# Performance work log

Measured on AMD Instinct MI355X. Metric: run time of the kernel, lower is better.

The kernel has to match this reference:

```python
import jax, jax.numpy as jnp
import numpy as np

B, S, D, H, DK, DV, SEG = 2, 4096, 1024, 8, 128, 128, 512
NSEG = S // SEG


def setup_inputs() -> dict:
    key = jax.random.key(0)
    k0, k1, k2, k3, k4, k5 = jax.random.split(key, 6)
    return {
        "x": jax.random.normal(k0, (B, S, D), jnp.float32),
        "Wk": jax.random.normal(k1, (H, D, DK), jnp.float32) / np.float32(np.sqrt(D)),
        "Wv": jax.random.normal(k2, (H, D, DV), jnp.float32) / np.float32(np.sqrt(D)),
        "Wq": jax.random.normal(k3, (H, D, DK), jnp.float32) / np.float32(np.sqrt(D)),
        "Wout": jax.random.normal(k4, (H * DV, D), jnp.float32) / np.float32(np.sqrt(H * DV)),
        "betas": jax.random.normal(k5, (1, H, 1, DV), jnp.float32),
    }


def reference(x, Wk, Wv, Wq, Wout, betas):
    # Per-head projections: (B,H,S,dk/dv)
    k_full = jnp.einsum('bsd,hdk->bhsk', x, Wk)
    v_full = jnp.einsum('bsd,hdk->bhsk', x, Wv)
    q_full = jnp.einsum('bsd,hdk->bhsk', x, Wq)

    def to_segs(t):  # (B,H,S,E) -> (NSEG,B,H,SEG,E)
        return t.reshape(B, H, NSEG, SEG, t.shape[-1]).transpose(2, 0, 1, 3, 4)

    segs = (to_segs(k_full), to_segs(v_full), to_segs(q_full))

    mem0 = jnp.zeros((B, H, DK, DV), x.dtype)           # compressive memory
    z0 = jnp.full((B, H, DK, 1), 1.0 / DK, x.dtype)     # normalizer
    causal_mask = jnp.tril(jnp.ones((SEG, SEG), bool))
    gate = jax.nn.sigmoid(betas)                        # (1,H,1,DV)
    scale = jnp.asarray(1.0 / np.sqrt(DK), x.dtype)

    def step(carry, seg):
        mem, z = carry
        k, v, q = seg                                   # (B,H,SEG,dk/dv)
        sigma_q = jax.nn.elu(q) + 1.0
        # segment-local causal softmax attention
        scores = jnp.einsum('bhik,bhjk->bhij', q, k) * scale
        scores = jnp.where(causal_mask, scores, -jnp.inf)
        att_dot = jax.nn.softmax(scores, axis=-1) @ v
        # linear-attention read from memory
        att_mem = (sigma_q @ mem) / (sigma_q @ z)
        # delta-rule memory update
        sigma_k = jax.nn.elu(k) + 1.0
        mem = mem + jnp.einsum('bhsk,bhsv->bhkv', sigma_k, v - (sigma_k @ mem) / (sigma_k @ z))
        z = z + jnp.sum(sigma_k, axis=-2, keepdims=True).swapaxes(-1, -2)
        # gated mix of memory and local attention
        att = gate * att_mem + (1.0 - gate) * att_dot   # (B,H,SEG,DV)
        att = att.transpose(0, 2, 1, 3).reshape(B, SEG, H * DV)
        return (mem, z), att @ Wout                     # (B,SEG,D)

    _, outs = jax.lax.scan(step, (mem0, z0), segs)      # (NSEG,B,SEG,D)
    return outs.transpose(1, 0, 2, 3).reshape(B, S, D)
```

## Files before the change

### kernel.cpp

```cpp
#include <hip/hip_runtime.h>

#define B_  2
#define S_  4096
#define D_  1024
#define H_  8
#define DK_ 128
#define DV_ 128
#define SEG_ 512
#define NSEG_ 8
#define BH_ 16
#define M_ 8192

typedef __attribute__((ext_vector_type(8))) short bf16x8;
typedef __attribute__((ext_vector_type(4))) float f32x4;

__device__ __forceinline__ float elu1(float x) { return x > 0.f ? x + 1.f : __expf(x); }
__device__ __forceinline__ float sigmoidf(float x) { return 1.f / (1.f + __expf(-x)); }

__device__ __forceinline__ unsigned short f2b(float f) {
    union { float f; unsigned int u; } x; x.f = f;
    unsigned int r = x.u + 0x7fffu + ((x.u >> 16) & 1u);
    return (unsigned short)(r >> 16);
}
__device__ __forceinline__ float b2f(unsigned short u) {
    union { unsigned int u; float f; } x; x.u = ((unsigned int)u) << 16; return x.f;
}

__device__ __forceinline__ void gl2lds16(const void* g, void* l) {
    __builtin_amdgcn_global_load_lds(
        (const __attribute__((address_space(1))) void*)g,
        (__attribute__((address_space(3))) void*)l, 16, 0, 0);
}

__global__ __launch_bounds__(256) void conv_bf16(
    const float* __restrict__ src, unsigned short* __restrict__ dst)
{
    int i = (blockIdx.x * 256 + threadIdx.x) * 4;
    float4 v = *(const float4*)(src + i);
    ushort4 o;
    o.x = f2b(v.x); o.y = f2b(v.y); o.z = f2b(v.z); o.w = f2b(v.w);
    *(ushort4*)(dst + i) = o;
}

__global__ __launch_bounds__(256) void transpose_conv(
    const float* __restrict__ src, unsigned short* __restrict__ dst, int R, int C)
{
    __shared__ float tile[32][33];
    const size_t moff = (size_t)blockIdx.z * R * C;
    src += moff; dst += moff;
    const int c0 = blockIdx.x * 32, r0 = blockIdx.y * 32;
    const int tx = threadIdx.x & 31, ty = threadIdx.x >> 5;
    #pragma unroll
    for (int i = 0; i < 32; i += 8)
        tile[ty + i][tx] = src[(size_t)(r0 + ty + i) * C + c0 + tx];
    __syncthreads();
    #pragma unroll
    for (int i = 0; i < 32; i += 8)
        dst[(size_t)(c0 + ty + i) * R + r0 + tx] = f2b(tile[tx][ty + i]);
}

__global__ __launch_bounds__(256) void colsum_k(
    const unsigned short* __restrict__ Kbb, float* __restrict__ colsum)
{
    __shared__ float red[32][128];
    const int t = threadIdx.x;
    const int bh = blockIdx.x >> 3, seg = blockIdx.x & 7;
    const unsigned short* Kp = Kbb + ((size_t)bh * 4096 + seg * 512) * 128;
    const int rbase = t >> 3, c0 = (t & 7) * 16;
    float part[16] = {};
    for (int chunk = 0; chunk < 16; ++chunk) {
        const unsigned short* p = Kp + (size_t)(chunk * 32 + rbase) * 128 + c0;
        bf16x8 a = *(const bf16x8*)p;
        bf16x8 b = *(const bf16x8*)(p + 8);
        #pragma unroll
        for (int j = 0; j < 8; ++j) {
            part[j]     += elu1(b2f((unsigned short)a[j]));
            part[j + 8] += elu1(b2f((unsigned short)b[j]));
        }
    }
    #pragma unroll
    for (int j = 0; j < 16; ++j) red[rbase][c0 + j] = part[j];
    __syncthreads();
    if (t < 128) {
        float s = 0.f;
        #pragma unroll
        for (int r = 0; r < 32; ++r) s += red[r][t];
        colsum[(size_t)blockIdx.x * 128 + t] = s;
    }
}

__global__ __launch_bounds__(256) void den_z(
    const unsigned short* __restrict__ Kbb, const float* __restrict__ colsum,
    float* __restrict__ den, float* __restrict__ zseg)
{
    __shared__ float zs[128];
    const int t = threadIdx.x;
    const int bh = blockIdx.x >> 3, seg = blockIdx.x & 7;
    if (t < 128) {
        float z = 1.f / 128.f;
        for (int j = 0; j < seg; ++j) z += colsum[(size_t)(bh * 8 + j) * 128 + t];
        zs[t] = z;
        zseg[(size_t)blockIdx.x * 128 + t] = z;
    }
    __syncthreads();
    #pragma unroll
    for (int rr = 0; rr < 2; ++rr) {
        int s = t + rr * 256;
        const unsigned short* kp = Kbb + ((size_t)bh * 4096 + seg * 512 + s) * 128;
        float d = 0.f;
        #pragma unroll 4
        for (int f = 0; f < 16; ++f) {
            bf16x8 a = *(const bf16x8*)(kp + f * 8);
            #pragma unroll
            for (int j = 0; j < 8; ++j)
                d += elu1(b2f((unsigned short)a[j])) * zs[f * 8 + j];
        }
        den[(size_t)bh * 4096 + seg * 512 + s] = d;
    }
}

__global__ __launch_bounds__(256) void sigma_kT2(
    const unsigned short* __restrict__ Kbb, const float* __restrict__ den,
    unsigned short* __restrict__ SkT, unsigned short* __restrict__ SkTs)
{
    __shared__ float tile[32][33];
    __shared__ float rden[32];
    const int bh = blockIdx.z;
    const int s0 = blockIdx.x * 32, dk0 = blockIdx.y * 32;
    const int tx = threadIdx.x & 31, ty = threadIdx.x >> 5;
    if (threadIdx.x < 32) rden[threadIdx.x] = 1.f / den[(size_t)bh * 4096 + s0 + threadIdx.x];
    #pragma unroll
    for (int i = 0; i < 32; i += 8)
        tile[ty + i][tx] = elu1(b2f(Kbb[((size_t)bh * 4096 + s0 + ty + i) * 128 + dk0 + tx]));
    __syncthreads();
    #pragma unroll
    for (int i = 0; i < 32; i += 8) {
        float v = tile[tx][ty + i];
        size_t o = ((size_t)bh * 128 + dk0 + ty + i) * 4096 + s0 + tx;
        SkT[o]  = f2b(v);
        SkTs[o] = f2b(v * rden[tx]);
    }
}

__device__ __forceinline__ void mfma_gemm_128(
    const unsigned short* __restrict__ A, int lda,
    const unsigned short* __restrict__ Bt, int ldb, int K,
    unsigned short* As, unsigned short* Bs, f32x4 acc[4][4])
{
    const int tid = threadIdx.x;
    const int wave = tid >> 6, lane = tid & 63;
    const int r4 = lane >> 2, c4 = (lane & 3) * 8;
    const int lrow = lane & 15, lquad = lane >> 4;
    const int wm = (wave >> 1) * 64, wn = (wave & 1) * 64;
    for (int k0 = 0; k0 < K; k0 += 32) {
        #pragma unroll
        for (int i = 0; i < 2; ++i) {
            int ar = wave * 32 + i * 16;
            gl2lds16(A  + (size_t)(ar + r4) * lda + k0 + c4, As + ar * 32);
            gl2lds16(Bt + (size_t)(ar + r4) * ldb + k0 + c4, Bs + ar * 32);
        }
        __syncthreads();
        bf16x8 af[4], bfr[4];
        #pragma unroll
        for (int i = 0; i < 4; ++i)
            af[i] = *(const bf16x8*)(As + (wm + i * 16 + lrow) * 32 + lquad * 8);
        #pragma unroll
        for (int j = 0; j < 4; ++j)
            bfr[j] = *(const bf16x8*)(Bs + (wn + j * 16 + lrow) * 32 + lquad * 8);
        #pragma unroll
        for (int i = 0; i < 4; ++i)
            #pragma unroll
            for (int j = 0; j < 4; ++j)
                acc[i][j] = __builtin_amdgcn_mfma_f32_16x16x32_bf16(af[i], bfr[j], acc[i][j], 0, 0, 0);
        __syncthreads();
    }
}

__global__ __launch_bounds__(256) void gemm_qkv_mfma(
    const unsigned short* __restrict__ xb, const unsigned short* __restrict__ Wtb,
    unsigned short* __restrict__ Qbb, unsigned short* __restrict__ Kbb,
    unsigned short* __restrict__ Vtb)
{
    __shared__ unsigned short As[128 * 32];
    __shared__ unsigned short Bs[128 * 32];
    const int m0 = blockIdx.x * 128;
    const int panel = blockIdx.y;
    const int which = panel >> 3, h = panel & 7;
    f32x4 acc[4][4] = {};
    mfma_gemm_128(xb + (size_t)m0 * 1024, 1024,
                  Wtb + (size_t)panel * 128 * 1024, 1024, 1024, As, Bs, acc);
    const int tid = threadIdx.x, wave = tid >> 6, lane = tid & 63;
    const int lrow = lane & 15, lquad = lane >> 4;
    const int wm = (wave >> 1) * 64, wn = (wave & 1) * 64;
    #pragma unroll
    for (int i = 0; i < 4; ++i)
        #pragma unroll
        for (int r = 0; r < 4; ++r) {
            int m = m0 + wm + i * 16 + lquad * 4 + r;
            int bb = m >> 12, s = m & 4095;
            int bh = bb * 8 + h;
            size_t rowbase = ((size_t)bh * 4096 + s) * 128;
            #pragma unroll
            for (int j = 0; j < 4; ++j) {
                int col = wn + j * 16 + lrow;
                unsigned short v = f2b(acc[i][j][r]);
                if (which == 0) Kbb[rowbase + col] = v;
                else if (which == 1)
                    Vtb[(((size_t)bh * 8 + (s >> 9)) * 128 + col) * 512 + (s & 511)] = v;
                else Qbb[rowbase + col] = v;
            }
        }
}

__global__ __launch_bounds__(256) void gemm_out_mfma(
    const unsigned short* __restrict__ A, const unsigned short* __restrict__ Bt,
    float* __restrict__ C)
{
    __shared__ unsigned short As[128 * 32];
    __shared__ unsigned short Bs[128 * 32];
    const int m0 = blockIdx.x * 128, n0 = blockIdx.y * 128;
    f32x4 acc[4][4] = {};
    mfma_gemm_128(A + (size_t)m0 * 1024, 1024,
                  Bt + (size_t)n0 * 1024, 1024, 1024, As, Bs, acc);
    const int tid = threadIdx.x, wave = tid >> 6, lane = tid & 63;
    const int lrow = lane & 15, lquad = lane >> 4;
    const int wm = (wave >> 1) * 64, wn = (wave & 1) * 64;
    #pragma unroll
    for (int i = 0; i < 4; ++i)
        #pragma unroll
        for (int r = 0; r < 4; ++r) {
            int m = m0 + wm + i * 16 + lquad * 4 + r;
            #pragma unroll
            for (int j = 0; j < 4; ++j)
                C[(size_t)m * 1024 + n0 + wn + j * 16 + lrow] = acc[i][j][r];
        }
}

__global__ __launch_bounds__(256) void ac_gemm(
    const unsigned short* __restrict__ SkT, const unsigned short* __restrict__ SkTs,
    const unsigned short* __restrict__ Vtb,
    unsigned short* __restrict__ Emat, float* __restrict__ Cmat)
{
    __shared__ unsigned short As[128 * 32];
    __shared__ unsigned short Bs1[128 * 32];
    __shared__ unsigned short Bs2[128 * 32];
    const int bh = blockIdx.x >> 3, seg = blockIdx.x & 7;
    const unsigned short* Ap  = SkT  + (size_t)bh * 128 * 4096 + seg * 512;
    const unsigned short* B1p = SkTs + (size_t)bh * 128 * 4096 + seg * 512;
    const unsigned short* B2p = Vtb  + (size_t)blockIdx.x * 128 * 512;
    const int tid = threadIdx.x;
    const int wave = tid >> 6, lane = tid & 63;
    const int r4 = lane >> 2, c4 = (lane & 3) * 8;
    const int lrow = lane & 15, lquad = lane >> 4;
    const int wm = (wave >> 1) * 64, wn = (wave & 1) * 64;
    f32x4 e[4][4] = {}, c[4][4] = {};
    for (int k0 = 0; k0 < 512; k0 += 32) {
        #pragma unroll
        for (int i = 0; i < 2; ++i) {
            int ar = wave * 32 + i * 16;
            gl2lds16(Ap  + (size_t)(ar + r4) * 4096 + k0 + c4, As  + ar * 32);
            gl2lds16(B1p + (size_t)(ar + r4) * 4096 + k0 + c4, Bs1 + ar * 32);
            gl2lds16(B2p + (size_t)(ar + r4) * 512  + k0 + c4, Bs2 + ar * 32);
        }
        __syncthreads();
        bf16x8 af[4], b1[4], b2[4];
        #pragma unroll
        for (int i = 0; i < 4; ++i)
            af[i] = *(const bf16x8*)(As + (wm + i * 16 + lrow) * 32 + lquad * 8);
        #pragma unroll
        for (int j = 0; j < 4; ++j) {
            b1[j] = *(const bf16x8*)(Bs1 + (wn + j * 16 + lrow) * 32 + lquad * 8);
            b2[j] = *(const bf16x8*)(Bs2 + (wn + j * 16 + lrow) * 32 + lquad * 8);
        }
        #pragma unroll
        for (int i = 0; i < 4; ++i)
            #pragma unroll
            for (int j = 0; j < 4; ++j) {
                e[i][j] = __builtin_amdgcn_mfma_f32_16x16x32_bf16(af[i], b1[j], e[i][j], 0, 0, 0);
                c[i][j] = __builtin_amdgcn_mfma_f32_16x16x32_bf16(af[i], b2[j], c[i][j], 0, 0, 0);
            }
        __syncthreads();
    }
    #pragma unroll
    for (int i = 0; i < 4; ++i)
        #pragma unroll
        for (int r = 0; r < 4; ++r) {
            int m = wm + i * 16 + lquad * 4 + r;
            #pragma unroll
            for (int j = 0; j < 4; ++j) {
                int nn = wn + j * 16 + lrow;
                size_t o = (size_t)blockIdx.x * 16384 + (size_t)m * 128 + nn;
                Emat[o] = f2b(-e[i][j][r]);
                Cmat[o] = c[i][j][r];
            }
        }
}

__global__ __launch_bounds__(512) void scan_step(
    const unsigned short* __restrict__ Emat, const float* __restrict__ Cmat,
    unsigned short* __restrict__ Memb)
{
    __shared__ unsigned short msh[128][136];
    const int t = threadIdx.x;
    const int wv = t >> 6, lane = t & 63;
    const int n16 = lane & 15, quad = lane >> 4;
    const int bh = blockIdx.x;
    f32x4 macc[8] = {};
    for (int seg = 0; seg < 8; ++seg) {
        unsigned short* gm = Memb + ((size_t)(bh * 8 + seg)) * 16384;
        #pragma unroll
        for (int vt = 0; vt < 8; ++vt) {
            ushort4 o;
            o.x = f2b(macc[vt][0]); o.y = f2b(macc[vt][1]);
            o.z = f2b(macc[vt][2]); o.w = f2b(macc[vt][3]);
            *(ushort4*)&msh[vt * 16 + n16][wv * 16 + quad * 4] = o;
            *(ushort4*)(gm + (size_t)(vt * 16 + n16) * 128 + wv * 16 + quad * 4) = o;
        }
        if (seg == 7) break;
        __syncthreads();
        const unsigned short* Ep = Emat + ((size_t)(bh * 8 + seg)) * 16384
                                 + (size_t)(wv * 16 + n16) * 128;
        bf16x8 ea[4];
        #pragma unroll
        for (int kf = 0; kf < 4; ++kf)
            ea[kf] = *(const bf16x8*)(Ep + kf * 32 + quad * 8);
        const float* Cp = Cmat + ((size_t)(bh * 8 + seg)) * 16384
                        + (size_t)(wv * 16 + quad * 4) * 128;
        #pragma unroll
        for (int vt = 0; vt < 8; ++vt)
            #pragma unroll
            for (int r = 0; r < 4; ++r)
                macc[vt][r] += Cp[(size_t)r * 128 + vt * 16 + n16];
        #pragma unroll
        for (int vt = 0; vt < 8; ++vt)
            #pragma unroll
            for (int kf = 0; kf < 4; ++kf) {
                bf16x8 bfr = *(const bf16x8*)&msh[vt * 16 + n16][kf * 32 + quad * 8];
                macc[vt] = __builtin_amdgcn_mfma_f32_16x16x32_bf16(ea[kf], bfr, macc[vt], 0, 0, 0);
            }
        __syncthreads();
    }
}

__global__ __launch_bounds__(256) void attn_out(
    const unsigned short* __restrict__ Qbb, const unsigned short* __restrict__ Kbb,
    const unsigned short* __restrict__ Vtb, const unsigned short* __restrict__ Memb,
    const float* __restrict__ zseg, const float* __restrict__ betas,
    unsigned short* __restrict__ Attb)
{
    __shared__ unsigned short Pl[4][16][72];
    const int tid = threadIdx.x, wave = tid >> 6, lane = tid & 63;
    const int n = lane & 15, quad = lane >> 4;
    const int bh = blockIdx.x >> 3, seg = blockIdx.x & 7, qt = blockIdx.y;
    const int b = bh >> 3, h = bh & 7;
    const float scale = 0.08838834764831845f;

    const unsigned short* Qp = Qbb + ((size_t)bh * 4096 + seg * 512 + qt * 64 + wave * 16) * 128;
    const unsigned short* Kp = Kbb + ((size_t)bh * 4096 + seg * 512) * 128;
    const unsigned short* Vp = Vtb + ((size_t)bh * 8 + seg) * 128 * 512;

    bf16x8 aQ[4];
    #pragma unroll
    for (int kc = 0; kc < 4; ++kc)
        aQ[kc] = *(const bf16x8*)(Qp + n * 128 + kc * 32 + quad * 8);

    f32x4 O[8] = {};
    float m_i[4], l_i[4];
    #pragma unroll
    for (int r = 0; r < 4; ++r) { m_i[r] = -1e30f; l_i[r] = 0.f; }

    for (int jt = 0; jt <= qt; ++jt) {
        f32x4 Sf[4] = {};
        #pragma unroll
        for (int kc = 0; kc < 4; ++kc) {
            bf16x8 bK[4];
            #pragma unroll
            for (int ns = 0; ns < 4; ++ns)
                bK[ns] = *(const bf16x8*)(Kp + (size_t)(jt * 64 + ns * 16 + n) * 128 + kc * 32 + quad * 8);
            #pragma unroll
            for (int ns = 0; ns < 4; ++ns)
                Sf[ns] = __builtin_amdgcn_mfma_f32_16x16x32_bf16(aQ[kc], bK[ns], Sf[ns], 0, 0, 0);
        }
        #pragma unroll
        for (int reg = 0; reg < 4; ++reg) {
            int grow = qt * 64 + wave * 16 + quad * 4 + reg;
            float sv[4];
            #pragma unroll
            for (int ns = 0; ns < 4; ++ns) {
                int gcol = jt * 64 + ns * 16 + n;
                sv[ns] = (gcol <= grow) ? Sf[ns][reg] * scale : -1e30f;
            }
            float mx = fmaxf(fmaxf(sv[0], sv[1]), fmaxf(sv[2], sv[3]));
            mx = fmaxf(mx, __shfl_xor(mx, 1));
            mx = fmaxf(mx, __shfl_xor(mx, 2));
            mx = fmaxf(mx, __shfl_xor(mx, 4));
            mx = fmaxf(mx, __shfl_xor(mx, 8));
            float mn = fmaxf(m_i[reg], mx);
            float alpha = __expf(m_i[reg] - mn);
            m_i[reg] = mn;
            float rs = 0.f;
            #pragma unroll
            for (int ns = 0; ns < 4; ++ns) {
                float p = __expf(sv[ns] - mn);
                rs += p;
                Pl[wave][quad * 4 + reg][ns * 16 + n] = f2b(p);
            }
            rs += __shfl_xor(rs, 1);
            rs += __shfl_xor(rs, 2);
            rs += __shfl_xor(rs, 4);
            rs += __shfl_xor(rs, 8);
            l_i[reg] = l_i[reg] * alpha + rs;
            #pragma unroll
            for (int dvs = 0; dvs < 8; ++dvs) O[dvs][reg] *= alpha;
        }
        __syncthreads();
        bf16x8 aP0 = *(const bf16x8*)&Pl[wave][n][quad * 8];
        bf16x8 aP1 = *(const bf16x8*)&Pl[wave][n][32 + quad * 8];
        #pragma unroll
        for (int dvs = 0; dvs < 8; ++dvs) {
            bf16x8 bV0 = *(const bf16x8*)(Vp + (size_t)(dvs * 16 + n) * 512 + jt * 64 + quad * 8);
            bf16x8 bV1 = *(const bf16x8*)(Vp + (size_t)(dvs * 16 + n) * 512 + jt * 64 + 32 + quad * 8);
            O[dvs] = __builtin_amdgcn_mfma_f32_16x16x32_bf16(aP0, bV0, O[dvs], 0, 0, 0);
            O[dvs] = __builtin_amdgcn_mfma_f32_16x16x32_bf16(aP1, bV1, O[dvs], 0, 0, 0);
        }
        __syncthreads();
    }
    const float* zp = zseg + (size_t)(bh * 8 + seg) * 128;
    float den = 0.f;
    bf16x8 aS[4];
    #pragma unroll
    for (int kc = 0; kc < 4; ++kc) {
        float4 z0 = *(const float4*)(zp + kc * 32 + quad * 8);
        float4 z1 = *(const float4*)(zp + kc * 32 + quad * 8 + 4);
        float zv[8] = {z0.x, z0.y, z0.z, z0.w, z1.x, z1.y, z1.z, z1.w};
        bf16x8 a;
        #pragma unroll
        for (int j = 0; j < 8; ++j) {
            float s = elu1(b2f((unsigned short)aQ[kc][j]));
            den += s * zv[j];
            a[j] = (short)f2b(s);
        }
        aS[kc] = a;
    }
    den += __shfl_xor(den, 16);
    den += __shfl_xor(den, 32);
    const unsigned short* Mp = Memb + (size_t)(bh * 8 + seg) * 16384;
    f32x4 Om[8] = {};
    #pragma unroll
    for (int dvs = 0; dvs < 8; ++dvs)
        #pragma unroll
        for (int kc = 0; kc < 4; ++kc) {
            bf16x8 bm = *(const bf16x8*)(Mp + (size_t)(dvs * 16 + n) * 128 + kc * 32 + quad * 8);
            Om[dvs] = __builtin_amdgcn_mfma_f32_16x16x32_bf16(aS[kc], bm, Om[dvs], 0, 0, 0);
        }
    float irm[4], inv[4];
    #pragma unroll
    for (int r = 0; r < 4; ++r) {
        irm[r] = 1.f / __shfl(den, quad * 4 + r);
        inv[r] = 1.f / l_i[r];
    }
    #pragma unroll
    for (int dvs = 0; dvs < 8; ++dvs) {
        int dv = dvs * 16 + n;
        float g = sigmoidf(betas[h * 128 + dv]);
        #pragma unroll
        for (int r = 0; r < 4; ++r) {
            int s = seg * 512 + qt * 64 + wave * 16 + quad * 4 + r;
            float val = g * Om[dvs][r] * irm[r] + (1.f - g) * O[dvs][r] * inv[r];
            Attb[((size_t)b * 4096 + s) * 1024 + h * 128 + dv] = f2b(val);
        }
    }
}

extern "C" void kernel_launch(void* const* d_in, const int* in_sizes, int n_in,
                              void* d_out, int out_size, void* d_ws, size_t ws_size,
                              hipStream_t stream) {
    const float* x     = (const float*)d_in[0];
    const float* Wk    = (const float*)d_in[1];
    const float* Wv    = (const float*)d_in[2];
    const float* Wq    = (const float*)d_in[3];
    const float* Wout  = (const float*)d_in[4];
    const float* betas = (const float*)d_in[5];
    float* out = (float*)d_out;

    unsigned short* Qbb  = (unsigned short*)d_ws;
    unsigned short* Kbb  = Qbb + 8388608;
    unsigned short* Vtb  = Kbb + 8388608;
    unsigned short* SkT  = Vtb + 8388608;
    unsigned short* SkTs = SkT + 8388608;
    unsigned short* Emat = SkTs + 8388608;
    unsigned short* Memb = Emat + 2097152;
    float* Cmat   = (float*)(Memb + 2097152);
    float* colsum = Cmat + 2097152;
    float* zseg   = colsum + 16384;
    float* den    = zseg + 16384;
    unsigned short* xb    = SkT;
    unsigned short* Wtb   = SkTs;
    unsigned short* Attb  = SkT;
    unsigned short* Woutb = SkTs;

    conv_bf16<<<8192, 256, 0, stream>>>(x, xb);
    transpose_conv<<<dim3(4, 32, 8), 256, 0, stream>>>(Wk, Wtb,               1024, 128);
    transpose_conv<<<dim3(4, 32, 8), 256, 0, stream>>>(Wv, Wtb +  8 * 131072, 1024, 128);
    transpose_conv<<<dim3(4, 32, 8), 256, 0, stream>>>(Wq, Wtb + 16 * 131072, 1024, 128);
    gemm_qkv_mfma<<<dim3(64, 24), 256, 0, stream>>>(xb, Wtb, Qbb, Kbb, Vtb);
    colsum_k<<<128, 256, 0, stream>>>(Kbb, colsum);
    den_z<<<128, 256, 0, stream>>>(Kbb, colsum, den, zseg);
    sigma_kT2<<<dim3(128, 4, 16), 256, 0, stream>>>(Kbb, den, SkT, SkTs);
    ac_gemm<<<128, 256, 0, stream>>>(SkT, SkTs, Vtb, Emat, Cmat);
    scan_step<<<16, 512, 0, stream>>>(Emat, Cmat, Memb);
    attn_out<<<dim3(128, 8), 256, 0, stream>>>(Qbb, Kbb, Vtb, Memb, zseg, betas, Attb);
    transpose_conv<<<dim3(32, 32, 1), 256, 0, stream>>>(Wout, Woutb, 1024, 1024);
    gemm_out_mfma<<<dim3(64, 8), 256, 0, stream>>>(Attb, Woutb, out);
}
```

Before: 408.0 us.

## Balance causal attention tiles across waves and drop redundant barriers and masking

```diff
diff --git a/kernel.cpp b/kernel.cpp
--- a/kernel.cpp
+++ b/kernel.cpp
@@ -351,11 +351,15 @@
     __shared__ unsigned short Pl[4][16][72];
     const int tid = threadIdx.x, wave = tid >> 6, lane = tid & 63;
     const int n = lane & 15, quad = lane >> 4;
-    const int bh = blockIdx.x >> 3, seg = blockIdx.x & 7, qt = blockIdx.y;
+    const int bh = blockIdx.x >> 3, seg = blockIdx.x & 7;
+    const int y = blockIdx.y;
+    const int a = y & 3, half = y >> 2;
+    const int qt = (wave < 2) ? a : 7 - a;
+    const int strip = half * 2 + (wave & 1);
     const int b = bh >> 3, h = bh & 7;
     const float scale = 0.08838834764831845f;
 
-    const unsigned short* Qp = Qbb + ((size_t)bh * 4096 + seg * 512 + qt * 64 + wave * 16) * 128;
+    const unsigned short* Qp = Qbb + ((size_t)bh * 4096 + seg * 512 + qt * 64 + strip * 16) * 128;
     const unsigned short* Kp = Kbb + ((size_t)bh * 4096 + seg * 512) * 128;
     const unsigned short* Vp = Vtb + ((size_t)bh * 8 + seg) * 128 * 512;
 
@@ -381,23 +385,28 @@
             for (int ns = 0; ns < 4; ++ns)
                 Sf[ns] = __builtin_amdgcn_mfma_f32_16x16x32_bf16(aQ[kc], bK[ns], Sf[ns], 0, 0, 0);
         }
+        const bool diag = (jt == qt);
         #pragma unroll
         for (int reg = 0; reg < 4; ++reg) {
-            int grow = qt * 64 + wave * 16 + quad * 4 + reg;
             float sv[4];
-            #pragma unroll
-            for (int ns = 0; ns < 4; ++ns) {
-                int gcol = jt * 64 + ns * 16 + n;
-                sv[ns] = (gcol <= grow) ? Sf[ns][reg] * scale : -1e30f;
+            if (diag) {
+                int grow = qt * 64 + strip * 16 + quad * 4 + reg;
+                #pragma unroll
+                for (int ns = 0; ns < 4; ++ns) {
+                    int gcol = jt * 64 + ns * 16 + n;
+                    sv[ns] = (gcol <= grow) ? Sf[ns][reg] * scale : -1e30f;
+                }
+            } else {
+                #pragma unroll
+                for (int ns = 0; ns < 4; ++ns) sv[ns] = Sf[ns][reg] * scale;
             }
             float mx = fmaxf(fmaxf(sv[0], sv[1]), fmaxf(sv[2], sv[3]));
             mx = fmaxf(mx, __shfl_xor(mx, 1));
             mx = fmaxf(mx, __shfl_xor(mx, 2));
             mx = fmaxf(mx, __shfl_xor(mx, 4));
             mx = fmaxf(mx, __shfl_xor(mx, 8));
+            unsigned long long grew = __ballot(mx > m_i[reg]);
             float mn = fmaxf(m_i[reg], mx);
-            float alpha = __expf(m_i[reg] - mn);
-            m_i[reg] = mn;
             float rs = 0.f;
             #pragma unroll
             for (int ns = 0; ns < 4; ++ns) {
@@ -409,11 +418,16 @@
             rs += __shfl_xor(rs, 2);
             rs += __shfl_xor(rs, 4);
             rs += __shfl_xor(rs, 8);
-            l_i[reg] = l_i[reg] * alpha + rs;
-            #pragma unroll
-            for (int dvs = 0; dvs < 8; ++dvs) O[dvs][reg] *= alpha;
-        }
-        __syncthreads();
+            if (grew) {
+                float alpha = __expf(m_i[reg] - mn);
+                m_i[reg] = mn;
+                l_i[reg] = l_i[reg] * alpha + rs;
+                #pragma unroll
+                for (int dvs = 0; dvs < 8; ++dvs) O[dvs][reg] *= alpha;
+            } else {
+                l_i[reg] += rs;
+            }
+        }
         bf16x8 aP0 = *(const bf16x8*)&Pl[wave][n][quad * 8];
         bf16x8 aP1 = *(const bf16x8*)&Pl[wave][n][32 + quad * 8];
         #pragma unroll
@@ -423,7 +437,6 @@
             O[dvs] = __builtin_amdgcn_mfma_f32_16x16x32_bf16(aP0, bV0, O[dvs], 0, 0, 0);
             O[dvs] = __builtin_amdgcn_mfma_f32_16x16x32_bf16(aP1, bV1, O[dvs], 0, 0, 0);
         }
-        __syncthreads();
     }
     const float* zp = zseg + (size_t)(bh * 8 + seg) * 128;
     float den = 0.f;
@@ -433,14 +446,14 @@
         float4 z0 = *(const float4*)(zp + kc * 32 + quad * 8);
         float4 z1 = *(const float4*)(zp + kc * 32 + quad * 8 + 4);
         float zv[8] = {z0.x, z0.y, z0.z, z0.w, z1.x, z1.y, z1.z, z1.w};
-        bf16x8 a;
+        bf16x8 aa;
         #pragma unroll
         for (int j = 0; j < 8; ++j) {
             float s = elu1(b2f((unsigned short)aQ[kc][j]));
             den += s * zv[j];
-            a[j] = (short)f2b(s);
-        }
-        aS[kc] = a;
+            aa[j] = (short)f2b(s);
+        }
+        aS[kc] = aa;
     }
     den += __shfl_xor(den, 16);
     den += __shfl_xor(den, 32);
@@ -465,7 +478,7 @@
         float g = sigmoidf(betas[h * 128 + dv]);
         #pragma unroll
         for (int r = 0; r < 4; ++r) {
-            int s = seg * 512 + qt * 64 + wave * 16 + quad * 4 + r;
+            int s = seg * 512 + qt * 64 + strip * 16 + quad * 4 + r;
             float val = g * Om[dvs][r] * irm[r] + (1.f - g) * O[dvs][r] * inv[r];
             Attb[((size_t)b * 4096 + s) * 1024 + h * 128 + dv] = f2b(val);
         }
```

Measured after the change: 404.1 us. Within noise of the previous version (-1.0%).
